# Kernel tuning notes

Hardware: AMD Instinct MI355X
Metric: run time of the kernel (lower is better)

The kernel has to match this reference:

```python
import jax, jax.numpy as jnp
import numpy as np

N_NODES = 100000
N_EDGES = 3200000
D_FEAT = 256
UNITS = 256


def setup_inputs() -> dict:
    key = jax.random.key(0)
    k1, k2, k3, k4, k5 = jax.random.split(key, 5)
    edge_row = jax.random.randint(k1, (N_EDGES,), 0, N_NODES, dtype=jnp.int32)
    edge_col = jax.random.randint(k2, (N_EDGES,), 0, N_NODES, dtype=jnp.int32)
    edge_val = jax.random.uniform(k3, (N_EDGES,), dtype=jnp.float32)
    x = jax.random.normal(k4, (N_NODES, D_FEAT), dtype=jnp.float32)
    weight = jax.random.normal(k5, (D_FEAT, UNITS), dtype=jnp.float32) * (1.0 / np.sqrt(D_FEAT))
    bias = jnp.zeros((UNITS,), dtype=jnp.float32)
    return {"edge_row": edge_row, "edge_col": edge_col, "edge_val": edge_val,
            "x": x, "weight": weight, "bias": bias}


def reference(edge_row, edge_col, edge_val, x, weight, bias):
    # h = X @ W  -- dense feature transform (N, units)
    h = x @ weight
    # out = An @ h -- SpMM over COO adjacency: out[r] += val_e * h[c_e]
    msgs = edge_val[:, None] * h[edge_col]          # (E, units) gather + scale
    out = jax.ops.segment_sum(msgs, edge_row, num_segments=N_NODES)
    out = out + bias
    return jax.nn.relu(out)
```

## Files before the change

### kernel.cpp

```cpp
#include <hip/hip_runtime.h>
#include <hip/hip_bf16.h>

#define N_NODES 100000
#define N_EDGES 3200000
#define DFEAT 256
#define UNITS 256

#define CHUNK 512
#define CHUNK_SHIFT 9
#define NCHUNKS ((N_NODES + CHUNK - 1) / CHUNK)

#define BIN_TILE 2048
#define BIN_NWG ((N_EDGES + BIN_TILE - 1) / BIN_TILE)
#define PADC 208

typedef short bf16x8 __attribute__((ext_vector_type(8)));
typedef float f32x4 __attribute__((ext_vector_type(4)));

__device__ __forceinline__ unsigned short f2bf(float f) {
    union { float f; unsigned u; } v; v.f = f;
    unsigned u = v.u;
    u += 0x7FFFu + ((u >> 16) & 1u);
    return (unsigned short)(u >> 16);
}

__global__ __launch_bounds__(256) void convert_xw(const float4* __restrict__ x4,
                                                  unsigned short* __restrict__ xh,
                                                  const float* __restrict__ w,
                                                  unsigned short* __restrict__ wt) {
    if (blockIdx.x < 25000) {
        size_t i = (size_t)blockIdx.x * 256 + threadIdx.x;
        float4 v = x4[i];
        ushort4 o = make_ushort4(f2bf(v.x), f2bf(v.y), f2bf(v.z), f2bf(v.w));
        *(ushort4*)&xh[i * 4] = o;
    } else {
        int n = blockIdx.x - 25000, k = threadIdx.x;
        wt[n * DFEAT + k] = f2bf(w[k * UNITS + n]);
    }
}

__global__ __launch_bounds__(256) void chunk_hist(const int* __restrict__ erow,
                                                  int* __restrict__ hist_all) {
    __shared__ int h[256];
    const int tid = threadIdx.x;
    h[tid] = 0;
    __syncthreads();
    const int base = blockIdx.x * BIN_TILE;
#pragma unroll
    for (int j = 0; j < 8; ++j) {
        int e = base + j * 256 + tid;
        if (e < N_EDGES) atomicAdd(&h[erow[e] >> CHUNK_SHIFT], 1);
    }
    __syncthreads();
    if (tid < NCHUNKS) hist_all[blockIdx.x * PADC + tid] = h[tid];
}

__global__ __launch_bounds__(256) void col_scan(int* __restrict__ hist_all,
                                                int* __restrict__ chunk_cnt) {
    __shared__ int t[256];
    const int b = blockIdx.x;
    const int tid = threadIdx.x;
    int v[7]; int local = 0;
#pragma unroll
    for (int j = 0; j < 7; ++j) {
        int w = tid * 7 + j;
        v[j] = (w < BIN_NWG) ? hist_all[w * PADC + b] : 0;
        local += v[j];
    }
    t[tid] = local;
    __syncthreads();
    for (int off = 1; off < 256; off <<= 1) {
        int u = 0;
        if (tid >= off) u = t[tid - off];
        __syncthreads();
        if (tid >= off) t[tid] += u;
        __syncthreads();
    }
    int run = t[tid] - local;
#pragma unroll
    for (int j = 0; j < 7; ++j) {
        int w = tid * 7 + j;
        if (w < BIN_NWG) { hist_all[w * PADC + b] = run; run += v[j]; }
    }
    if (tid == 255) chunk_cnt[b] = t[255];
}

__global__ void scan_chunks(const int* __restrict__ chunk_cnt, int* __restrict__ csum) {
    __shared__ int t[256];
    const int tid = threadIdx.x;
    int v = (tid < NCHUNKS) ? chunk_cnt[tid] : 0;
    t[tid] = v;
    __syncthreads();
    for (int off = 1; off < 256; off <<= 1) {
        int u = 0;
        if (tid >= off) u = t[tid - off];
        __syncthreads();
        if (tid >= off) t[tid] += u;
        __syncthreads();
    }
    if (tid < NCHUNKS) csum[tid] = t[tid] - v;
}

__global__ __launch_bounds__(256) void bin_edges(const int* __restrict__ erow,
                                                 const int* __restrict__ ecol,
                                                 const float* __restrict__ eval,
                                                 const int* __restrict__ hist_all,
                                                 const int* __restrict__ csum,
                                                 uint2* __restrict__ bin) {
    __shared__ int hist[256];
    __shared__ int scnt[256];
    __shared__ int delta[256];
    __shared__ uint2 rec[BIN_TILE];
    const int tid = threadIdx.x;
    const int base = blockIdx.x * BIN_TILE;

    hist[tid] = 0;
    __syncthreads();

    int r[8]; unsigned pk[8];
#pragma unroll
    for (int j = 0; j < 8; ++j) {
        int e = base + j * 256 + tid;
        if (e < N_EDGES) {
            r[j] = erow[e];
            pk[j] = (((unsigned)ecol[e]) << 15) | (f2bf(eval[e]) & 0x7FFFu);
            atomicAdd(&hist[r[j] >> CHUNK_SHIFT], 1);
        } else {
            r[j] = -1;
        }
    }
    __syncthreads();

    const int cntb = hist[tid];
    for (int off = 1; off < 256; off <<= 1) {
        int u = 0;
        if (tid >= off) u = hist[tid - off];
        __syncthreads();
        if (tid >= off) hist[tid] += u;
        __syncthreads();
    }
    const int excl = hist[tid] - cntb;
    if (tid < NCHUNKS)
        delta[tid] = csum[tid] + hist_all[blockIdx.x * PADC + tid] - excl;
    scnt[tid] = 0;
    __syncthreads();

#pragma unroll
    for (int j = 0; j < 8; ++j) {
        if (r[j] >= 0) {
            int b = r[j] >> CHUNK_SHIFT;
            int s = (b ? hist[b - 1] : 0) + atomicAdd(&scnt[b], 1);
            rec[s] = make_uint2(pk[j], (unsigned)r[j]);
        }
    }
    __syncthreads();

    const int n = min(BIN_TILE, N_EDGES - base);
    for (int s = tid; s < n; s += 256) {
        uint2 q = rec[s];
        bin[delta[(int)q.y >> CHUNK_SHIFT] + s] = q;
    }
}

__global__ __launch_bounds__(512) void sort_chunk(const int* __restrict__ csum,
                                                  const uint2* __restrict__ bin,
                                                  int* __restrict__ row_ptr,
                                                  unsigned* __restrict__ cv) {
    __shared__ int h[CHUNK];
    const int b = blockIdx.x;
    const int tid = threadIdx.x;
    const int start = csum[b];
    const int end = (b + 1 < NCHUNKS) ? csum[b + 1] : N_EDGES;

    h[tid] = 0;
    __syncthreads();
    {
        int i = start + tid;
        for (; i + 3 * 512 < end; i += 4 * 512) {
            int r0 = (int)bin[i].y, r1 = (int)bin[i + 512].y;
            int r2 = (int)bin[i + 1024].y, r3 = (int)bin[i + 1536].y;
            atomicAdd(&h[r0 & (CHUNK - 1)], 1);
            atomicAdd(&h[r1 & (CHUNK - 1)], 1);
            atomicAdd(&h[r2 & (CHUNK - 1)], 1);
            atomicAdd(&h[r3 & (CHUNK - 1)], 1);
        }
        for (; i < end; i += 512)
            atomicAdd(&h[(int)bin[i].y & (CHUNK - 1)], 1);
    }
    __syncthreads();

    const int cnt = h[tid];
    for (int off = 1; off < 512; off <<= 1) {
        int u = 0;
        if (tid >= off) u = h[tid - off];
        __syncthreads();
        if (tid >= off) h[tid] += u;
        __syncthreads();
    }
    const int rp = start + h[tid] - cnt;
    const int row = (b << CHUNK_SHIFT) + tid;
    if (row < N_NODES) row_ptr[row] = rp;
    if (b == NCHUNKS - 1 && tid == 0) row_ptr[N_NODES] = N_EDGES;
    __syncthreads();
    h[tid] = rp;
    __syncthreads();

    int i = start + tid;
    for (; i + 3 * 512 < end; i += 4 * 512) {
        uint2 q0 = bin[i], q1 = bin[i + 512], q2 = bin[i + 1024], q3 = bin[i + 1536];
        int p0 = atomicAdd(&h[(int)q0.y & (CHUNK - 1)], 1);
        int p1 = atomicAdd(&h[(int)q1.y & (CHUNK - 1)], 1);
        int p2 = atomicAdd(&h[(int)q2.y & (CHUNK - 1)], 1);
        int p3 = atomicAdd(&h[(int)q3.y & (CHUNK - 1)], 1);
        cv[p0] = q0.x; cv[p1] = q1.x; cv[p2] = q2.x; cv[p3] = q3.x;
    }
    for (; i < end; i += 512) {
        uint2 q = bin[i];
        int p = atomicAdd(&h[(int)q.y & (CHUNK - 1)], 1);
        cv[p] = q.x;
    }
}

__global__ __launch_bounds__(256) void gather_rows(const int* __restrict__ row_ptr,
                                                   const unsigned* __restrict__ cv,
                                                   const unsigned short* __restrict__ xh,
                                                   unsigned short* __restrict__ tmp) {
    const int row = blockIdx.x * 4 + (threadIdx.x >> 6);
    if (row >= N_NODES) return;
    const int lane = threadIdx.x & 63;
    const int start = row_ptr[row];
    const int deg = row_ptr[row + 1] - start;
    const unsigned* __restrict__ p = cv + start;
    const uint2* __restrict__ x2 = (const uint2*)xh;

    float a0 = 0.f, a1 = 0.f, a2 = 0.f, a3 = 0.f;
    int i = 0;
    for (; i + 7 < deg; i += 8) {
        unsigned e[8]; uint2 g[8];
#pragma unroll
        for (int j = 0; j < 8; ++j) e[j] = p[i + j];
#pragma unroll
        for (int j = 0; j < 8; ++j) g[j] = x2[(size_t)(e[j] >> 15) * 64 + lane];
#pragma unroll
        for (int j = 0; j < 8; ++j) {
            float v = __uint_as_float((e[j] & 0x7FFFu) << 16);
            a0 = fmaf(v, __uint_as_float(g[j].x << 16), a0);
            a1 = fmaf(v, __uint_as_float(g[j].x & 0xFFFF0000u), a1);
            a2 = fmaf(v, __uint_as_float(g[j].y << 16), a2);
            a3 = fmaf(v, __uint_as_float(g[j].y & 0xFFFF0000u), a3);
        }
    }
    for (; i + 3 < deg; i += 4) {
        unsigned e[4]; uint2 g[4];
#pragma unroll
        for (int j = 0; j < 4; ++j) e[j] = p[i + j];
#pragma unroll
        for (int j = 0; j < 4; ++j) g[j] = x2[(size_t)(e[j] >> 15) * 64 + lane];
#pragma unroll
        for (int j = 0; j < 4; ++j) {
            float v = __uint_as_float((e[j] & 0x7FFFu) << 16);
            a0 = fmaf(v, __uint_as_float(g[j].x << 16), a0);
            a1 = fmaf(v, __uint_as_float(g[j].x & 0xFFFF0000u), a1);
            a2 = fmaf(v, __uint_as_float(g[j].y << 16), a2);
            a3 = fmaf(v, __uint_as_float(g[j].y & 0xFFFF0000u), a3);
        }
    }
    for (; i < deg; ++i) {
        unsigned e0 = p[i];
        uint2 g0 = x2[(size_t)(e0 >> 15) * 64 + lane];
        float v0 = __uint_as_float((e0 & 0x7FFFu) << 16);
        a0 = fmaf(v0, __uint_as_float(g0.x << 16), a0);
        a1 = fmaf(v0, __uint_as_float(g0.x & 0xFFFF0000u), a1);
        a2 = fmaf(v0, __uint_as_float(g0.y << 16), a2);
        a3 = fmaf(v0, __uint_as_float(g0.y & 0xFFFF0000u), a3);
    }
    ushort4 o = make_ushort4(f2bf(a0), f2bf(a1), f2bf(a2), f2bf(a3));
    *(ushort4*)&tmp[(size_t)row * 256 + lane * 4] = o;
}

#define GBM 64
#define LDK2 264

__global__ __launch_bounds__(256) void gemm_mfma(
    const unsigned short* __restrict__ A,
    const unsigned short* __restrict__ Bt,
    const float* __restrict__ bias,
    float* __restrict__ C, int M)
{
    __shared__ unsigned short As[GBM * LDK2];

    const int tid = threadIdx.x;
    const int lane = tid & 63;
    const int wave_n = tid >> 6;
    const int block_m = blockIdx.x * GBM;

    const int quad = lane >> 4;
    const int l16 = lane & 15;

    {
        const int ar = tid >> 2;
        const int seg = tid & 3;
        const int gm = block_m + ar;
        uint4 v[8] = {};
        if (gm < M) {
            const uint4* src = (const uint4*)(A + (size_t)gm * DFEAT + seg * 64);
#pragma unroll
            for (int j = 0; j < 8; ++j) v[j] = src[j];
        }
        uint4* dst = (uint4*)&As[ar * LDK2 + seg * 64];
#pragma unroll
        for (int j = 0; j < 8; ++j) dst[j] = v[j];
    }
    __syncthreads();

    f32x4 acc[4][4];
#pragma unroll
    for (int i = 0; i < 4; ++i)
#pragma unroll
        for (int j = 0; j < 4; ++j)
            acc[i][j] = {0.f, 0.f, 0.f, 0.f};

#pragma unroll
    for (int ks = 0; ks < 8; ++ks) {
        const int ko = ks * 32 + quad * 8;
        bf16x8 af[4], bfr[4];
#pragma unroll
        for (int i = 0; i < 4; ++i)
            af[i] = *(const bf16x8*)&As[(i * 16 + l16) * LDK2 + ko];
#pragma unroll
        for (int j = 0; j < 4; ++j)
            bfr[j] = *(const bf16x8*)&Bt[(size_t)(wave_n * 64 + j * 16 + l16) * DFEAT + ko];
#pragma unroll
        for (int i = 0; i < 4; ++i)
#pragma unroll
            for (int j = 0; j < 4; ++j)
                acc[i][j] = __builtin_amdgcn_mfma_f32_16x16x32_bf16(
                    af[i], bfr[j], acc[i][j], 0, 0, 0);
    }

#pragma unroll
    for (int j = 0; j < 4; ++j) {
        const int n = wave_n * 64 + j * 16 + l16;
        const float bj = bias[n];
#pragma unroll
        for (int i = 0; i < 4; ++i) {
            const int m0 = block_m + i * 16 + quad * 4;
#pragma unroll
            for (int rg = 0; rg < 4; ++rg) {
                const int m = m0 + rg;
                if (m < M)
                    C[(size_t)m * UNITS + n] = fmaxf(acc[i][j][rg] + bj, 0.f);
            }
        }
    }
}

extern "C" void kernel_launch(void* const* d_in, const int* in_sizes, int n_in,
                              void* d_out, int out_size, void* d_ws, size_t ws_size,
                              hipStream_t stream) {
    const int*   erow = (const int*)d_in[0];
    const int*   ecol = (const int*)d_in[1];
    const float* eval = (const float*)d_in[2];
    const float* x    = (const float*)d_in[3];
    const float* w    = (const float*)d_in[4];
    const float* bias = (const float*)d_in[5];
    float* out = (float*)d_out;

    char* ws = (char*)d_ws;
    unsigned short* tmp       = (unsigned short*)(ws);
    int*            row_ptr   = (int*)(ws + 51200000);
    int*            csum      = (int*)(ws + 51600016);
    int*            chunk_cnt = (int*)(ws + 51601040);
    unsigned*       cv        = (unsigned*)(ws + 51602064);
    unsigned short* wt        = (unsigned short*)(ws + 64402064);
    uint2*          bin       = (uint2*)(ws + 64533136);
    int*            hist_all  = (int*)(ws + 90133136);

    unsigned short* xh = (unsigned short*)d_out;

    convert_xw<<<25000 + UNITS, 256, 0, stream>>>((const float4*)x, xh, w, wt);

    chunk_hist<<<BIN_NWG, 256, 0, stream>>>(erow, hist_all);
    col_scan<<<NCHUNKS, 256, 0, stream>>>(hist_all, chunk_cnt);
    scan_chunks<<<1, 256, 0, stream>>>(chunk_cnt, csum);
    bin_edges<<<BIN_NWG, 256, 0, stream>>>(erow, ecol, eval, hist_all, csum, bin);
    sort_chunk<<<NCHUNKS, 512, 0, stream>>>(csum, bin, row_ptr, cv);

    gather_rows<<<(N_NODES + 3) / 4, 256, 0, stream>>>(row_ptr, cv, xh, tmp);

    gemm_mfma<<<(N_NODES + GBM - 1) / GBM, 256, 0, stream>>>(tmp, wt, bias, out, N_NODES);
}
```

Measured before the change: 555.4 us.

## Fuse gather and GEMM via shared memory; merge histogram into convert kernel

The row gather/SpMM now writes its bf16 aggregated rows straight into shared memory, and an MFMA GEMM in the same workgroup consumes them. This removes the 51 MB bf16 intermediate write and its re-read, and drops one kernel launch. The chunk histogram is folded into the x/W conversion launch as extra workgroups, so those independent jobs overlap. In exchange, the GEMM tile shrinks to 32 rows with 2x2 MFMA per wave, which reloads weights from global more often. The xh buffer also moves from the output to the workspace.

Measured after the change: 511.9 us. -7.8%, faster.

```diff
diff --git a/kernel.cpp b/kernel.cpp
--- a/kernel.cpp
+++ b/kernel.cpp
@@ -24,35 +24,35 @@
     return (unsigned short)(u >> 16);
 }
 
-__global__ __launch_bounds__(256) void convert_xw(const float4* __restrict__ x4,
-                                                  unsigned short* __restrict__ xh,
-                                                  const float* __restrict__ w,
-                                                  unsigned short* __restrict__ wt) {
+__global__ __launch_bounds__(256) void convert_hist(const float4* __restrict__ x4,
+                                                    unsigned short* __restrict__ xh,
+                                                    const float* __restrict__ w,
+                                                    unsigned short* __restrict__ wt,
+                                                    const int* __restrict__ erow,
+                                                    int* __restrict__ hist_all) {
     if (blockIdx.x < 25000) {
         size_t i = (size_t)blockIdx.x * 256 + threadIdx.x;
         float4 v = x4[i];
         ushort4 o = make_ushort4(f2bf(v.x), f2bf(v.y), f2bf(v.z), f2bf(v.w));
         *(ushort4*)&xh[i * 4] = o;
-    } else {
+    } else if (blockIdx.x < 25256) {
         int n = blockIdx.x - 25000, k = threadIdx.x;
         wt[n * DFEAT + k] = f2bf(w[k * UNITS + n]);
-    }
-}
-
-__global__ __launch_bounds__(256) void chunk_hist(const int* __restrict__ erow,
-                                                  int* __restrict__ hist_all) {
-    __shared__ int h[256];
-    const int tid = threadIdx.x;
-    h[tid] = 0;
-    __syncthreads();
-    const int base = blockIdx.x * BIN_TILE;
-#pragma unroll
-    for (int j = 0; j < 8; ++j) {
-        int e = base + j * 256 + tid;
-        if (e < N_EDGES) atomicAdd(&h[erow[e] >> CHUNK_SHIFT], 1);
-    }
-    __syncthreads();
-    if (tid < NCHUNKS) hist_all[blockIdx.x * PADC + tid] = h[tid];
+    } else {
+        __shared__ int h[256];
+        const int wg = blockIdx.x - 25256;
+        const int tid = threadIdx.x;
+        h[tid] = 0;
+        __syncthreads();
+        const int base = wg * BIN_TILE;
+#pragma unroll
+        for (int j = 0; j < 8; ++j) {
+            int e = base + j * 256 + tid;
+            if (e < N_EDGES) atomicAdd(&h[erow[e] >> CHUNK_SHIFT], 1);
+        }
+        __syncthreads();
+        if (tid < NCHUNKS) hist_all[wg * PADC + tid] = h[tid];
+    }
 }
 
 __global__ __launch_bounds__(256) void col_scan(int* __restrict__ hist_all,
@@ -221,135 +221,118 @@
     }
 }
 
-__global__ __launch_bounds__(256) void gather_rows(const int* __restrict__ row_ptr,
-                                                   const unsigned* __restrict__ cv,
-                                                   const unsigned short* __restrict__ xh,
-                                                   unsigned short* __restrict__ tmp) {
-    const int row = blockIdx.x * 4 + (threadIdx.x >> 6);
-    if (row >= N_NODES) return;
-    const int lane = threadIdx.x & 63;
-    const int start = row_ptr[row];
-    const int deg = row_ptr[row + 1] - start;
-    const unsigned* __restrict__ p = cv + start;
-    const uint2* __restrict__ x2 = (const uint2*)xh;
-
-    float a0 = 0.f, a1 = 0.f, a2 = 0.f, a3 = 0.f;
-    int i = 0;
-    for (; i + 7 < deg; i += 8) {
-        unsigned e[8]; uint2 g[8];
-#pragma unroll
-        for (int j = 0; j < 8; ++j) e[j] = p[i + j];
-#pragma unroll
-        for (int j = 0; j < 8; ++j) g[j] = x2[(size_t)(e[j] >> 15) * 64 + lane];
-#pragma unroll
-        for (int j = 0; j < 8; ++j) {
-            float v = __uint_as_float((e[j] & 0x7FFFu) << 16);
-            a0 = fmaf(v, __uint_as_float(g[j].x << 16), a0);
-            a1 = fmaf(v, __uint_as_float(g[j].x & 0xFFFF0000u), a1);
-            a2 = fmaf(v, __uint_as_float(g[j].y << 16), a2);
-            a3 = fmaf(v, __uint_as_float(g[j].y & 0xFFFF0000u), a3);
-        }
-    }
-    for (; i + 3 < deg; i += 4) {
-        unsigned e[4]; uint2 g[4];
-#pragma unroll
-        for (int j = 0; j < 4; ++j) e[j] = p[i + j];
-#pragma unroll
-        for (int j = 0; j < 4; ++j) g[j] = x2[(size_t)(e[j] >> 15) * 64 + lane];
-#pragma unroll
-        for (int j = 0; j < 4; ++j) {
-            float v = __uint_as_float((e[j] & 0x7FFFu) << 16);
-            a0 = fmaf(v, __uint_as_float(g[j].x << 16), a0);
-            a1 = fmaf(v, __uint_as_float(g[j].x & 0xFFFF0000u), a1);
-            a2 = fmaf(v, __uint_as_float(g[j].y << 16), a2);
-            a3 = fmaf(v, __uint_as_float(g[j].y & 0xFFFF0000u), a3);
-        }
-    }
-    for (; i < deg; ++i) {
-        unsigned e0 = p[i];
-        uint2 g0 = x2[(size_t)(e0 >> 15) * 64 + lane];
-        float v0 = __uint_as_float((e0 & 0x7FFFu) << 16);
-        a0 = fmaf(v0, __uint_as_float(g0.x << 16), a0);
-        a1 = fmaf(v0, __uint_as_float(g0.x & 0xFFFF0000u), a1);
-        a2 = fmaf(v0, __uint_as_float(g0.y << 16), a2);
-        a3 = fmaf(v0, __uint_as_float(g0.y & 0xFFFF0000u), a3);
-    }
-    ushort4 o = make_ushort4(f2bf(a0), f2bf(a1), f2bf(a2), f2bf(a3));
-    *(ushort4*)&tmp[(size_t)row * 256 + lane * 4] = o;
-}
-
-#define GBM 64
-#define LDK2 264
-
-__global__ __launch_bounds__(256) void gemm_mfma(
-    const unsigned short* __restrict__ A,
+#define FB 32
+#define FLD 264
+
+__global__ __launch_bounds__(512) void gather_gemm(
+    const int* __restrict__ row_ptr,
+    const unsigned* __restrict__ cv,
+    const unsigned short* __restrict__ xh,
     const unsigned short* __restrict__ Bt,
     const float* __restrict__ bias,
-    float* __restrict__ C, int M)
+    float* __restrict__ C)
 {
-    __shared__ unsigned short As[GBM * LDK2];
+    __shared__ unsigned short As[FB * FLD];
 
     const int tid = threadIdx.x;
     const int lane = tid & 63;
-    const int wave_n = tid >> 6;
-    const int block_m = blockIdx.x * GBM;
+    const int wv = tid >> 6;
+    const int block_m = blockIdx.x * FB;
+    const uint2* __restrict__ x2 = (const uint2*)xh;
+
+#pragma unroll
+    for (int rr = 0; rr < 4; ++rr) {
+        const int rl = wv * 4 + rr;
+        const int row = block_m + rl;
+        const int start = row_ptr[row];
+        const int deg = row_ptr[row + 1] - start;
+        const unsigned* __restrict__ p = cv + start;
+
+        float a0 = 0.f, a1 = 0.f, a2 = 0.f, a3 = 0.f;
+        int i = 0;
+        for (; i + 7 < deg; i += 8) {
+            unsigned e[8]; uint2 g[8];
+#pragma unroll
+            for (int j = 0; j < 8; ++j) e[j] = p[i + j];
+#pragma unroll
+            for (int j = 0; j < 8; ++j) g[j] = x2[(size_t)(e[j] >> 15) * 64 + lane];
+#pragma unroll
+            for (int j = 0; j < 8; ++j) {
+                float v = __uint_as_float((e[j] & 0x7FFFu) << 16);
+                a0 = fmaf(v, __uint_as_float(g[j].x << 16), a0);
+                a1 = fmaf(v, __uint_as_float(g[j].x & 0xFFFF0000u), a1);
+                a2 = fmaf(v, __uint_as_float(g[j].y << 16), a2);
+                a3 = fmaf(v, __uint_as_float(g[j].y & 0xFFFF0000u), a3);
+            }
+        }
+        for (; i + 3 < deg; i += 4) {
+            unsigned e[4]; uint2 g[4];
+#pragma unroll
+            for (int j = 0; j < 4; ++j) e[j] = p[i + j];
+#pragma unroll
+            for (int j = 0; j < 4; ++j) g[j] = x2[(size_t)(e[j] >> 15) * 64 + lane];
+#pragma unroll
+            for (int j = 0; j < 4; ++j) {
+                float v = __uint_as_float((e[j] & 0x7FFFu) << 16);
+                a0 = fmaf(v, __uint_as_float(g[j].x << 16), a0);
+                a1 = fmaf(v, __uint_as_float(g[j].x & 0xFFFF0000u), a1);
+                a2 = fmaf(v, __uint_as_float(g[j].y << 16), a2);
+                a3 = fmaf(v, __uint_as_float(g[j].y & 0xFFFF0000u), a3);
+            }
+        }
+        for (; i < deg; ++i) {
+            unsigned e0 = p[i];
+            uint2 g0 = x2[(size_t)(e0 >> 15) * 64 + lane];
+            float v0 = __uint_as_float((e0 & 0x7FFFu) << 16);
+            a0 = fmaf(v0, __uint_as_float(g0.x << 16), a0);
+            a1 = fmaf(v0, __uint_as_float(g0.x & 0xFFFF0000u), a1);
+            a2 = fmaf(v0, __uint_as_float(g0.y << 16), a2);
+            a3 = fmaf(v0, __uint_as_float(g0.y & 0xFFFF0000u), a3);
+        }
+        ushort4 o = make_ushort4(f2bf(a0), f2bf(a1), f2bf(a2), f2bf(a3));
+        *(ushort4*)&As[rl * FLD + lane * 4] = o;
+    }
+    __syncthreads();
 
     const int quad = lane >> 4;
     const int l16 = lane & 15;
 
-    {
-        const int ar = tid >> 2;
-        const int seg = tid & 3;
-        const int gm = block_m + ar;
-        uint4 v[8] = {};
-        if (gm < M) {
-            const uint4* src = (const uint4*)(A + (size_t)gm * DFEAT + seg * 64);
-#pragma unroll
-            for (int j = 0; j < 8; ++j) v[j] = src[j];
-        }
-        uint4* dst = (uint4*)&As[ar * LDK2 + seg * 64];
-#pragma unroll
-        for (int j = 0; j < 8; ++j) dst[j] = v[j];
-    }
-    __syncthreads();
-
-    f32x4 acc[4][4];
-#pragma unroll
-    for (int i = 0; i < 4; ++i)
-#pragma unroll
-        for (int j = 0; j < 4; ++j)
+    f32x4 acc[2][2];
+#pragma unroll
+    for (int i = 0; i < 2; ++i)
+#pragma unroll
+        for (int j = 0; j < 2; ++j)
             acc[i][j] = {0.f, 0.f, 0.f, 0.f};
 
 #pragma unroll
     for (int ks = 0; ks < 8; ++ks) {
         const int ko = ks * 32 + quad * 8;
-        bf16x8 af[4], bfr[4];
-#pragma unroll
-        for (int i = 0; i < 4; ++i)
-            af[i] = *(const bf16x8*)&As[(i * 16 + l16) * LDK2 + ko];
-#pragma unroll
-        for (int j = 0; j < 4; ++j)
-            bfr[j] = *(const bf16x8*)&Bt[(size_t)(wave_n * 64 + j * 16 + l16) * DFEAT + ko];
-#pragma unroll
-        for (int i = 0; i < 4; ++i)
-#pragma unroll
-            for (int j = 0; j < 4; ++j)
+        bf16x8 af[2], bfr[2];
+#pragma unroll
+        for (int i = 0; i < 2; ++i)
+            af[i] = *(const bf16x8*)&As[(i * 16 + l16) * FLD + ko];
+#pragma unroll
+        for (int j = 0; j < 2; ++j)
+            bfr[j] = *(const bf16x8*)&Bt[(size_t)(wv * 32 + j * 16 + l16) * DFEAT + ko];
+#pragma unroll
+        for (int i = 0; i < 2; ++i)
+#pragma unroll
+            for (int j = 0; j < 2; ++j)
                 acc[i][j] = __builtin_amdgcn_mfma_f32_16x16x32_bf16(
                     af[i], bfr[j], acc[i][j], 0, 0, 0);
     }
 
 #pragma unroll
-    for (int j = 0; j < 4; ++j) {
-        const int n = wave_n * 64 + j * 16 + l16;
+    for (int j = 0; j < 2; ++j) {
+        const int n = wv * 32 + j * 16 + l16;
         const float bj = bias[n];
 #pragma unroll
-        for (int i = 0; i < 4; ++i) {
+        for (int i = 0; i < 2; ++i) {
             const int m0 = block_m + i * 16 + quad * 4;
 #pragma unroll
             for (int rg = 0; rg < 4; ++rg) {
                 const int m = m0 + rg;
-                if (m < M)
-                    C[(size_t)m * UNITS + n] = fmaxf(acc[i][j][rg] + bj, 0.f);
+                C[(size_t)m * UNITS + n] = fmaxf(acc[i][j][rg] + bj, 0.f);
             }
         }
     }
@@ -367,7 +350,7 @@
     float* out = (float*)d_out;
 
     char* ws = (char*)d_ws;
-    unsigned short* tmp       = (unsigned short*)(ws);
+    unsigned short* xh        = (unsigned short*)(ws);
     int*            row_ptr   = (int*)(ws + 51200000);
     int*            csum      = (int*)(ws + 51600016);
     int*            chunk_cnt = (int*)(ws + 51601040);
@@ -376,17 +359,13 @@
     uint2*          bin       = (uint2*)(ws + 64533136);
     int*            hist_all  = (int*)(ws + 90133136);
 
-    unsigned short* xh = (unsigned short*)d_out;
-
-    convert_xw<<<25000 + UNITS, 256, 0, stream>>>((const float4*)x, xh, w, wt);
-
-    chunk_hist<<<BIN_NWG, 256, 0, stream>>>(erow, hist_all);
+    convert_hist<<<25000 + UNITS + BIN_NWG, 256, 0, stream>>>(
+        (const float4*)x, xh, w, wt, erow, hist_all);
+
     col_scan<<<NCHUNKS, 256, 0, stream>>>(hist_all, chunk_cnt);
     scan_chunks<<<1, 256, 0, stream>>>(chunk_cnt, csum);
     bin_edges<<<BIN_NWG, 256, 0, stream>>>(erow, ecol, eval, hist_all, csum, bin);
     sort_chunk<<<NCHUNKS, 512, 0, stream>>>(csum, bin, row_ptr, cv);
 
-    gather_rows<<<(N_NODES + 3) / 4, 256, 0, stream>>>(row_ptr, cv, xh, tmp);
-
-    gemm_mfma<<<(N_NODES + GBM - 1) / GBM, 256, 0, stream>>>(tmp, wt, bias, out, N_NODES);
-}
+    gather_gemm<<<N_NODES / FB, 512, 0, stream>>>(row_ptr, cv, xh, wt, bias, out);
+}
```
